# Kernel optimization log

Measured on AMD Instinct MI355X. Metric: run time of the kernel, lower is better.

## Reference

```python
import jax, jax.numpy as jnp
import numpy as np

B, N, D = 8, 8192, 128   # D = in_dim + out_dim
H, KQ = 8, 64


def setup_inputs() -> dict:
    key = jax.random.key(0)
    k1, k2, k3, k4 = jax.random.split(key, 4)
    std = 0.02
    x = jax.random.normal(k1, (B, N, D), dtype=jnp.float32)
    # torch Linear weights are [out_features, in_features]
    Wk = jax.random.normal(k2, (H, KQ, D), dtype=jnp.float32) * std
    Wq = jax.random.normal(k3, (H, KQ, D), dtype=jnp.float32) * std
    Wv = jax.random.normal(k4, (H, D, D), dtype=jnp.float32) * std
    return {"x": x, "Wk": Wk, "Wq": Wq, "Wv": Wv}


def reference(x, Wk, Wq, Wv):
    # Per-head linear projections (Linear: y = x @ W^T), batched over heads.
    K = jnp.einsum('bnd,hkd->bhnk', x, Wk)   # [B,H,N,KQ]
    Q = jnp.einsum('bnd,hkd->bhnk', x, Wq)   # [B,H,N,KQ]
    V = jnp.einsum('bnd,hed->bhne', x, Wv)   # [B,H,N,D]
    # No softmax => (Q K^T) V == Q (K^T V): associative reorder avoids the
    # O(N^2) score matrix while computing identical math.
    KtV = jnp.einsum('bhnk,bhne->bhke', K, V)      # [B,H,KQ,D]
    out = jnp.einsum('bhnk,bhke->bne', Q, KtV)     # heads summed, [B,N,D]
    return out
```

## Files before the change

kernel.cpp:

```cpp
#include <hip/hip_runtime.h>
#include <hip/hip_bf16.h>

#define BB 8
#define NN 8192
#define DD 128
#define HH 8
#define KQ 64
#define SPLIT 64
#define NPB (NN / SPLIT)

typedef __attribute__((ext_vector_type(8))) short s16x8;
typedef __attribute__((ext_vector_type(4))) float f32x4;
typedef __attribute__((ext_vector_type(4))) unsigned short u16x4;
typedef __attribute__((ext_vector_type(8))) unsigned short u16x8;

__device__ __forceinline__ unsigned short bfr(float f) {
  unsigned u = __builtin_bit_cast(unsigned, f);
  u += 0x7fffu + ((u >> 16) & 1u);
  return (unsigned short)(u >> 16);
}
__device__ __forceinline__ float b2f(unsigned short u) {
  unsigned v = (unsigned)u << 16;
  return __builtin_bit_cast(float, v);
}

__global__ __launch_bounds__(256) void prep(
    const float* __restrict__ Wk, const float* __restrict__ Wq,
    const float* __restrict__ Wv, unsigned short* __restrict__ Wkbf,
    unsigned short* __restrict__ Wvbf, unsigned short* __restrict__ Wqt) {
  const int bx = blockIdx.x, t = threadIdx.x;
  if (bx < 64) {
    const int i = bx * 1024 + t * 4;
    float4 v = *(const float4*)(Wk + i);
    u16x4 o = {bfr(v.x), bfr(v.y), bfr(v.z), bfr(v.w)};
    *(u16x4*)(Wkbf + i) = o;
  } else if (bx < 192) {
    const int i = (bx - 64) * 1024 + t * 4;
    float4 v = *(const float4*)(Wv + i);
    u16x4 o = {bfr(v.x), bfr(v.y), bfr(v.z), bfr(v.w)};
    *(u16x4*)(Wvbf + i) = o;
  } else {
    const int h = bx - 192;
    const int d4 = (t & 31) * 4;
#pragma unroll
    for (int p = 0; p < 8; ++p) {
      const int k = (t >> 5) + p * 8;
      float4 v = *(const float4*)(Wq + (size_t)h * 8192 + k * DD + d4);
      unsigned short* dst = Wqt + (size_t)h * 8192;
      dst[(d4 + 0) * KQ + k] = bfr(v.x);
      dst[(d4 + 1) * KQ + k] = bfr(v.y);
      dst[(d4 + 2) * KQ + k] = bfr(v.z);
      dst[(d4 + 3) * KQ + k] = bfr(v.w);
    }
  }
}

__global__ __launch_bounds__(256) void gram_mfma(
    const float* __restrict__ x, unsigned short* __restrict__ part) {
  const int s = blockIdx.x, b = blockIdx.y;
  const int t = threadIdx.x, l = t & 63, w = t >> 6;
  __shared__ __align__(16) unsigned short xt[2][128 * 32];
  const float* xb = x + ((size_t)b * NN + (size_t)s * NPB) * DD;

  const int sd = t & 15;
  const int sn = (t >> 4) * 2;

  f32x4 acc[4][4];
#pragma unroll
  for (int i = 0; i < 4; ++i)
#pragma unroll
    for (int j = 0; j < 4; ++j) acc[i][j] = (f32x4){0.f, 0.f, 0.f, 0.f};

  float rv[8][2];
  auto load = [&](int sub) {
    const float* xs = xb + (size_t)sub * 32 * DD;
#pragma unroll
    for (int i = 0; i < 8; ++i)
#pragma unroll
      for (int j = 0; j < 2; ++j)
        rv[i][j] = xs[(size_t)(sn + j) * DD + sd + 16 * i];
  };
  auto stage = [&](int buf) {
    const int slot = sn >> 3;
#pragma unroll
    for (int i = 0; i < 8; ++i) {
      const int d = sd + 16 * i;
      unsigned v = (unsigned)bfr(rv[i][0]) | ((unsigned)bfr(rv[i][1]) << 16);
      char* dst = (char*)&xt[buf][0] + d * 64 +
                  (((slot ^ ((d >> 1) & 3)) << 4) | ((sn & 7) * 2));
      *(unsigned*)dst = v;
    }
  };

  load(0);
  stage(0);
  __syncthreads();

  const int d1s = (w & 1) * 64, d2s = (w >> 1) * 64;
  const int lr = l & 15, lk = l >> 4;
  const int nsub = NPB / 32;

  for (int sub = 0; sub < nsub; ++sub) {
    const int cur = sub & 1;
    if (sub + 1 < nsub) load(sub + 1);
    {
      s16x8 af[4], bv[4];
#pragma unroll
      for (int i = 0; i < 4; ++i) {
        const int row = d1s + i * 16 + lr;
        af[i] = *(const s16x8*)((const char*)&xt[cur][0] + row * 64 +
                                ((lk ^ ((row >> 1) & 3)) << 4));
      }
#pragma unroll
      for (int j = 0; j < 4; ++j) {
        const int row = d2s + j * 16 + lr;
        bv[j] = *(const s16x8*)((const char*)&xt[cur][0] + row * 64 +
                                ((lk ^ ((row >> 1) & 3)) << 4));
      }
#pragma unroll
      for (int i = 0; i < 4; ++i)
#pragma unroll
        for (int j = 0; j < 4; ++j)
          acc[i][j] =
              __builtin_amdgcn_mfma_f32_16x16x32_bf16(af[i], bv[j], acc[i][j], 0, 0, 0);
    }
    if (sub + 1 < nsub) stage(cur ^ 1);
    __syncthreads();
  }

  unsigned short* gdst = part + (((size_t)b * SPLIT + s) << 14);
#pragma unroll
  for (int i = 0; i < 4; ++i)
#pragma unroll
    for (int j = 0; j < 4; ++j) {
      u16x4 o = {bfr(acc[i][j][0]), bfr(acc[i][j][1]),
                 bfr(acc[i][j][2]), bfr(acc[i][j][3])};
      *(u16x4*)(gdst + ((w * 16 + i * 4 + j) * 64 + l) * 4) = o;
    }
}

__global__ __launch_bounds__(256) void gram_reduce(
    const unsigned short* __restrict__ part, unsigned short* __restrict__ Gbf) {
  const int b = blockIdx.y;
  const int fidx = blockIdx.x * 1024 + threadIdx.x * 4;
  const unsigned short* p = part + ((size_t)b * SPLIT << 14) + fidx;
  float s0 = 0.f, s1 = 0.f, s2 = 0.f, s3 = 0.f;
  for (int i = 0; i < SPLIT; ++i) {
    u16x4 v = *(const u16x4*)(p + ((size_t)i << 14));
    s0 += b2f(v[0]); s1 += b2f(v[1]); s2 += b2f(v[2]); s3 += b2f(v[3]);
  }
  const int q = fidx >> 2;
  const int l = q & 63, u = q >> 6;
  const int j = u & 3, i = (u >> 2) & 3, w = u >> 4;
  const int lr = l & 15, lk = l >> 4;
  const int row0 = (w & 1) * 64 + i * 16 + lk * 4;
  const int col = (w >> 1) * 64 + j * 16 + lr;
  unsigned short* g = Gbf + ((size_t)b << 14);
  g[(row0 + 0) * 128 + col] = bfr(s0);
  g[(row0 + 1) * 128 + col] = bfr(s1);
  g[(row0 + 2) * 128 + col] = bfr(s2);
  g[(row0 + 3) * 128 + col] = bfr(s3);
}

__global__ __launch_bounds__(256) void middle_fused(
    const unsigned short* __restrict__ Gbf, const unsigned short* __restrict__ Wkbf,
    const unsigned short* __restrict__ Wvbf, const unsigned short* __restrict__ Wqt,
    float* __restrict__ Mp) {
  const int b = blockIdx.x >> 3, h = blockIdx.x & 7;
  const int t = threadIdx.x, l = t & 63, w = t >> 6;
  const int lr = l & 15, lk = l >> 4;
  __shared__ __align__(16) unsigned short Gs[128 * 128];
  __shared__ __align__(16) unsigned short T1s[64 * 128];
  __shared__ __align__(16) unsigned short T2t[128 * 64];

  const unsigned short* gsrc = Gbf + ((size_t)b << 14);
#pragma unroll
  for (int c8 = 0; c8 < 8; ++c8) {
    const int c = t + c8 * 256;
    const int row = c >> 4, slot = c & 15;
    u16x8 v = *(const u16x8*)(gsrc + row * 128 + slot * 8);
    *(u16x8*)(&Gs[row * 128 + ((slot ^ (row & 15)) << 3)]) = v;
  }
  __syncthreads();

  const unsigned short* wk = Wkbf + ((size_t)h << 13);
  s16x8 aw[4];
#pragma unroll
  for (int ks = 0; ks < 4; ++ks)
    aw[ks] = *(const s16x8*)(wk + ((w * 16 + lr) << 7) + ks * 32 + lk * 8);
  f32x4 accA[8];
#pragma unroll
  for (int j = 0; j < 8; ++j) accA[j] = (f32x4){0.f, 0.f, 0.f, 0.f};
#pragma unroll
  for (int nj = 0; nj < 8; ++nj)
#pragma unroll
    for (int ks = 0; ks < 4; ++ks) {
      const int row = nj * 16 + lr;
      const int slot = (ks * 4 + lk) ^ (row & 15);
      s16x8 bfrag = *(const s16x8*)(&Gs[(row << 7) + (slot << 3)]);
      accA[nj] = __builtin_amdgcn_mfma_f32_16x16x32_bf16(aw[ks], bfrag, accA[nj], 0, 0, 0);
    }
#pragma unroll
  for (int nj = 0; nj < 8; ++nj)
#pragma unroll
    for (int r = 0; r < 4; ++r) {
      const int row = w * 16 + lk * 4 + r;
      const int col = nj * 16 + lr;
      const int slot = (col >> 3) ^ (row & 15);
      T1s[(row << 7) + (slot << 3) + (col & 7)] = bfr(accA[nj][r]);
    }
  __syncthreads();

  s16x8 a2[4];
#pragma unroll
  for (int ks = 0; ks < 4; ++ks) {
    const int row = w * 16 + lr;
    const int slot = (ks * 4 + lk) ^ (row & 15);
    a2[ks] = *(const s16x8*)(&T1s[(row << 7) + (slot << 3)]);
  }
  const unsigned short* wv = Wvbf + ((size_t)h << 14);
  f32x4 accB[8];
#pragma unroll
  for (int j = 0; j < 8; ++j) accB[j] = (f32x4){0.f, 0.f, 0.f, 0.f};
#pragma unroll
  for (int nj = 0; nj < 8; ++nj)
#pragma unroll
    for (int ks = 0; ks < 4; ++ks) {
      s16x8 bfrag = *(const s16x8*)(wv + (((size_t)(nj * 16 + lr)) << 7) + ks * 32 + lk * 8);
      accB[nj] = __builtin_amdgcn_mfma_f32_16x16x32_bf16(a2[ks], bfrag, accB[nj], 0, 0, 0);
    }
#pragma unroll
  for (int nj = 0; nj < 8; ++nj)
#pragma unroll
    for (int r = 0; r < 4; ++r) {
      const int e = nj * 16 + lr;
      const int k = w * 16 + lk * 4 + r;
      const int slot = (k >> 3) ^ (e & 7);
      T2t[(e << 6) + (slot << 3) + (k & 7)] = bfr(accB[nj][r]);
    }
  __syncthreads();

  const unsigned short* wq = Wqt + ((size_t)h << 13);
  float* mp = Mp + (((size_t)(b * 8 + h)) << 14);
#pragma unroll
  for (int p = 0; p < 2; ++p) {
    s16x8 a3[2];
#pragma unroll
    for (int ks = 0; ks < 2; ++ks) {
      const int row = (2 * w + p) * 16 + lr;
      const int slot = (ks * 4 + lk) ^ (row & 7);
      a3[ks] = *(const s16x8*)(&T2t[(row << 6) + (slot << 3)]);
    }
    f32x4 accC[8];
#pragma unroll
    for (int j = 0; j < 8; ++j) accC[j] = (f32x4){0.f, 0.f, 0.f, 0.f};
#pragma unroll
    for (int nj = 0; nj < 8; ++nj)
#pragma unroll
      for (int ks = 0; ks < 2; ++ks) {
        s16x8 bfrag = *(const s16x8*)(wq + ((nj * 16 + lr) << 6) + ks * 32 + lk * 8);
        accC[nj] = __builtin_amdgcn_mfma_f32_16x16x32_bf16(a3[ks], bfrag, accC[nj], 0, 0, 0);
      }
#pragma unroll
    for (int nj = 0; nj < 8; ++nj)
#pragma unroll
      for (int r = 0; r < 4; ++r) {
        const int row = (2 * w + p) * 16 + lk * 4 + r;
        const int col = nj * 16 + lr;
        mp[(row << 7) + col] = accC[nj][r];
      }
  }
}

__global__ __launch_bounds__(256) void m_reduce_t(
    const float* __restrict__ Mp, unsigned short* __restrict__ Mt) {
  const int b = blockIdx.y;
  const int idx = blockIdx.x * 1024 + threadIdx.x * 4;
  float4 s = {0.f, 0.f, 0.f, 0.f};
#pragma unroll
  for (int h = 0; h < 8; ++h) {
    float4 v = *(const float4*)(Mp + (((size_t)(b * 8 + h)) << 14) + idx);
    s.x += v.x; s.y += v.y; s.z += v.z; s.w += v.w;
  }
  u16x4 o = {bfr(s.x), bfr(s.y), bfr(s.z), bfr(s.w)};
  *(u16x4*)(Mt + ((size_t)b << 14) + idx) = o;
}

__global__ __launch_bounds__(256) void out_mfma(
    const float* __restrict__ x, const unsigned short* __restrict__ Mt,
    float* __restrict__ out) {
  const int b = blockIdx.y, t = threadIdx.x, l = t & 63, w = t >> 6;
  const int r0 = blockIdx.x * 64;
  __shared__ __align__(16) unsigned short mt[DD * DD];
  const unsigned short* msrc = Mt + (size_t)b * (DD * DD);
#pragma unroll
  for (int k = 0; k < 8; ++k) {
    const int c = t + k * 256;
    const int e = c >> 4, slot = c & 15;
    u16x8 v = *(const u16x8*)(msrc + e * DD + slot * 8);
    *(u16x8*)(&mt[e * DD + ((slot ^ (e & 15)) << 3)]) = v;
  }
  __syncthreads();

  const int lr = l & 15, lk = l >> 4;
  const int rw = r0 + w * 16;
  f32x4 acc[8];
#pragma unroll
  for (int j = 0; j < 8; ++j) acc[j] = (f32x4){0.f, 0.f, 0.f, 0.f};

  const float* xb = x + (size_t)b * NN * DD;
#pragma unroll
  for (int ks = 0; ks < 4; ++ks) {
    const float* p = xb + (size_t)(rw + lr) * DD + ks * 32 + lk * 8;
    float4 v0 = *(const float4*)p;
    float4 v1 = *(const float4*)(p + 4);
    s16x8 af;
    af[0] = (short)bfr(v0.x); af[1] = (short)bfr(v0.y);
    af[2] = (short)bfr(v0.z); af[3] = (short)bfr(v0.w);
    af[4] = (short)bfr(v1.x); af[5] = (short)bfr(v1.y);
    af[6] = (short)bfr(v1.z); af[7] = (short)bfr(v1.w);
    const int slot = ks * 4 + lk;
#pragma unroll
    for (int j = 0; j < 8; ++j) {
      const int e = j * 16 + lr;
      s16x8 bv = *(const s16x8*)(&mt[e * DD + ((slot ^ (e & 15)) << 3)]);
      acc[j] = __builtin_amdgcn_mfma_f32_16x16x32_bf16(af, bv, acc[j], 0, 0, 0);
    }
  }

  float* ob = out + (size_t)b * NN * DD;
#pragma unroll
  for (int j = 0; j < 8; ++j)
#pragma unroll
    for (int r = 0; r < 4; ++r) {
      const int row = rw + lk * 4 + r;
      const int col = j * 16 + lr;
      ob[(size_t)row * DD + col] = acc[j][r];
    }
}

extern "C" void kernel_launch(void* const* d_in, const int* in_sizes, int n_in,
                              void* d_out, int out_size, void* d_ws, size_t ws_size,
                              hipStream_t stream) {
  const float* x  = (const float*)d_in[0];
  const float* Wk = (const float*)d_in[1];
  const float* Wq = (const float*)d_in[2];
  const float* Wv = (const float*)d_in[3];
  float* out = (float*)d_out;
  float* ws  = (float*)d_ws;

  const size_t off_Mp   = 0;
  const size_t off_part = off_Mp + (size_t)BB * HH * DD * DD;
  const size_t off_Gbf  = off_part + (size_t)BB * SPLIT * DD * DD / 2;
  const size_t off_Mt   = off_Gbf + (size_t)BB * DD * DD / 2;
  const size_t off_Wkbf = off_Mt + (size_t)BB * DD * DD / 2;
  const size_t off_Wvbf = off_Wkbf + (size_t)HH * KQ * DD / 2;
  const size_t off_Wqt  = off_Wvbf + (size_t)HH * DD * DD / 2;

  float* Mp   = ws + off_Mp;
  unsigned short* part = (unsigned short*)(ws + off_part);
  unsigned short* Gbf  = (unsigned short*)(ws + off_Gbf);
  unsigned short* Mt   = (unsigned short*)(ws + off_Mt);
  unsigned short* Wkbf = (unsigned short*)(ws + off_Wkbf);
  unsigned short* Wvbf = (unsigned short*)(ws + off_Wvbf);
  unsigned short* Wqt  = (unsigned short*)(ws + off_Wqt);

  gram_mfma<<<dim3(SPLIT, BB), 256, 0, stream>>>(x, part);
  prep<<<200, 256, 0, stream>>>(Wk, Wq, Wv, Wkbf, Wvbf, Wqt);
  gram_reduce<<<dim3(16, BB), 256, 0, stream>>>(part, Gbf);
  middle_fused<<<64, 256, 0, stream>>>(Gbf, Wkbf, Wvbf, Wqt, Mp);
  m_reduce_t<<<dim3(16, BB), 256, 0, stream>>>(Mp, Mt);
  out_mfma<<<dim3(NN / 64, BB), 256, 0, stream>>>(x, Mt, out);
}
```

Baseline: 52.11 us.

## Fuse gram reduce with weight prep, deepen gram prefetch, drop LDS in out kernel

Three changes are made. Gram partial reduction and weight bf16 conversion are merged into one launch to save a kernel launch. The gram kernel's global loads are prefetched two sub-tiles ahead with a fully unrolled loop to hide memory latency. The output kernel now reads the M matrix straight from global/L2 instead of staging it in LDS, and uses 128-thread blocks covering 32 rows, which removes the LDS fill and barrier but relies on cache for repeated B-fragment loads and adds register pressure in the gram kernel.

After: 57.56 us. 1.1x slower.

```diff
diff --git a/kernel.cpp b/kernel.cpp
--- a/kernel.cpp
+++ b/kernel.cpp
@@ -24,27 +24,147 @@
   return __builtin_bit_cast(float, v);
 }
 
-__global__ __launch_bounds__(256) void prep(
+__global__ __launch_bounds__(256) void gram_mfma(
+    const float* __restrict__ x, unsigned short* __restrict__ part) {
+  const int s = blockIdx.x, b = blockIdx.y;
+  const int t = threadIdx.x, l = t & 63, w = t >> 6;
+  __shared__ __align__(16) unsigned short xt[2][128 * 32];
+  const float* xb = x + ((size_t)b * NN + (size_t)s * NPB) * DD;
+
+  const int sd = t & 15;
+  const int sn = (t >> 4) * 2;
+
+  f32x4 acc[4][4];
+#pragma unroll
+  for (int i = 0; i < 4; ++i)
+#pragma unroll
+    for (int j = 0; j < 4; ++j) acc[i][j] = (f32x4){0.f, 0.f, 0.f, 0.f};
+
+  float rv[2][8][2];
+  auto load = [&](int slot2, int sub) {
+    const float* xs = xb + (size_t)sub * 32 * DD;
+#pragma unroll
+    for (int i = 0; i < 8; ++i)
+#pragma unroll
+      for (int j = 0; j < 2; ++j)
+        rv[slot2][i][j] = xs[(size_t)(sn + j) * DD + sd + 16 * i];
+  };
+  auto stage = [&](int buf, int slot2) {
+    const int slot = sn >> 3;
+#pragma unroll
+    for (int i = 0; i < 8; ++i) {
+      const int d = sd + 16 * i;
+      unsigned v = (unsigned)bfr(rv[slot2][i][0]) |
+                   ((unsigned)bfr(rv[slot2][i][1]) << 16);
+      char* dst = (char*)&xt[buf][0] + d * 64 +
+                  (((slot ^ ((d >> 1) & 3)) << 4) | ((sn & 7) * 2));
+      *(unsigned*)dst = v;
+    }
+  };
+
+  const int nsub = NPB / 32;
+  load(0, 0);
+  load(1, 1);
+  stage(0, 0);
+  __syncthreads();
+
+  const int d1s = (w & 1) * 64, d2s = (w >> 1) * 64;
+  const int lr = l & 15, lk = l >> 4;
+
+#pragma unroll
+  for (int sub = 0; sub < nsub; ++sub) {
+    const int cur = sub & 1;
+    if (sub + 2 < nsub) load(sub & 1, sub + 2);
+    {
+      s16x8 af[4], bv[4];
+#pragma unroll
+      for (int i = 0; i < 4; ++i) {
+        const int row = d1s + i * 16 + lr;
+        af[i] = *(const s16x8*)((const char*)&xt[cur][0] + row * 64 +
+                                ((lk ^ ((row >> 1) & 3)) << 4));
+      }
+#pragma unroll
+      for (int j = 0; j < 4; ++j) {
+        const int row = d2s + j * 16 + lr;
+        bv[j] = *(const s16x8*)((const char*)&xt[cur][0] + row * 64 +
+                                ((lk ^ ((row >> 1) & 3)) << 4));
+      }
+#pragma unroll
+      for (int i = 0; i < 4; ++i)
+#pragma unroll
+        for (int j = 0; j < 4; ++j)
+          acc[i][j] =
+              __builtin_amdgcn_mfma_f32_16x16x32_bf16(af[i], bv[j], acc[i][j], 0, 0, 0);
+    }
+    if (sub + 1 < nsub) stage(cur ^ 1, (sub + 1) & 1);
+    __syncthreads();
+  }
+
+  unsigned short* gdst = part + (((size_t)b * SPLIT + s) << 14);
+#pragma unroll
+  for (int i = 0; i < 4; ++i)
+#pragma unroll
+    for (int j = 0; j < 4; ++j) {
+      u16x4 o = {bfr(acc[i][j][0]), bfr(acc[i][j][1]),
+                 bfr(acc[i][j][2]), bfr(acc[i][j][3])};
+      *(u16x4*)(gdst + ((w * 16 + i * 4 + j) * 64 + l) * 4) = o;
+    }
+}
+
+__global__ __launch_bounds__(256) void redprep(
+    const unsigned short* __restrict__ part, unsigned short* __restrict__ Gbf,
     const float* __restrict__ Wk, const float* __restrict__ Wq,
     const float* __restrict__ Wv, unsigned short* __restrict__ Wkbf,
     unsigned short* __restrict__ Wvbf, unsigned short* __restrict__ Wqt) {
-  const int bx = blockIdx.x, t = threadIdx.x;
-  if (bx < 64) {
-    const int i = bx * 1024 + t * 4;
-    float4 v = *(const float4*)(Wk + i);
-    u16x4 o = {bfr(v.x), bfr(v.y), bfr(v.z), bfr(v.w)};
-    *(u16x4*)(Wkbf + i) = o;
-  } else if (bx < 192) {
-    const int i = (bx - 64) * 1024 + t * 4;
-    float4 v = *(const float4*)(Wv + i);
-    u16x4 o = {bfr(v.x), bfr(v.y), bfr(v.z), bfr(v.w)};
-    *(u16x4*)(Wvbf + i) = o;
+  const int bx = blockIdx.x, by = blockIdx.y, t = threadIdx.x;
+  if (bx < 16) {
+    const int b = by;
+    const int fidx = bx * 1024 + t * 4;
+    const unsigned short* p = part + ((size_t)b * SPLIT << 14) + fidx;
+    float s0 = 0.f, s1 = 0.f, s2 = 0.f, s3 = 0.f;
+    for (int i = 0; i < SPLIT; ++i) {
+      u16x4 v = *(const u16x4*)(p + ((size_t)i << 14));
+      s0 += b2f(v[0]); s1 += b2f(v[1]); s2 += b2f(v[2]); s3 += b2f(v[3]);
+    }
+    const int q = fidx >> 2;
+    const int l = q & 63, u = q >> 6;
+    const int j = u & 3, i = (u >> 2) & 3, w = u >> 4;
+    const int lr = l & 15, lk = l >> 4;
+    const int row0 = (w & 1) * 64 + i * 16 + lk * 4;
+    const int col = (w >> 1) * 64 + j * 16 + lr;
+    unsigned short* g = Gbf + ((size_t)b << 14);
+    g[(row0 + 0) * 128 + col] = bfr(s0);
+    g[(row0 + 1) * 128 + col] = bfr(s1);
+    g[(row0 + 2) * 128 + col] = bfr(s2);
+    g[(row0 + 3) * 128 + col] = bfr(s3);
+    return;
+  }
+  const int c = (bx - 16) * 8 + by;
+  if (c < 16) {
+    const int base = c * 4096;
+#pragma unroll
+    for (int q = 0; q < 4; ++q) {
+      const int i = base + q * 1024 + t * 4;
+      float4 v = *(const float4*)(Wk + i);
+      u16x4 o = {bfr(v.x), bfr(v.y), bfr(v.z), bfr(v.w)};
+      *(u16x4*)(Wkbf + i) = o;
+    }
+  } else if (c < 48) {
+    const int base = (c - 16) * 4096;
+#pragma unroll
+    for (int q = 0; q < 4; ++q) {
+      const int i = base + q * 1024 + t * 4;
+      float4 v = *(const float4*)(Wv + i);
+      u16x4 o = {bfr(v.x), bfr(v.y), bfr(v.z), bfr(v.w)};
+      *(u16x4*)(Wvbf + i) = o;
+    }
   } else {
-    const int h = bx - 192;
+    const int c2 = c - 48;
+    const int h = c2 >> 1, piece = c2 & 1;
     const int d4 = (t & 31) * 4;
 #pragma unroll
-    for (int p = 0; p < 8; ++p) {
-      const int k = (t >> 5) + p * 8;
+    for (int p = 0; p < 4; ++p) {
+      const int k = piece * 32 + (t >> 5) * 4 + p;
       float4 v = *(const float4*)(Wq + (size_t)h * 8192 + k * DD + d4);
       unsigned short* dst = Wqt + (size_t)h * 8192;
       dst[(d4 + 0) * KQ + k] = bfr(v.x);
@@ -53,113 +173,6 @@
       dst[(d4 + 3) * KQ + k] = bfr(v.w);
     }
   }
-}
-
-__global__ __launch_bounds__(256) void gram_mfma(
-    const float* __restrict__ x, unsigned short* __restrict__ part) {
-  const int s = blockIdx.x, b = blockIdx.y;
-  const int t = threadIdx.x, l = t & 63, w = t >> 6;
-  __shared__ __align__(16) unsigned short xt[2][128 * 32];
-  const float* xb = x + ((size_t)b * NN + (size_t)s * NPB) * DD;
-
-  const int sd = t & 15;
-  const int sn = (t >> 4) * 2;
-
-  f32x4 acc[4][4];
-#pragma unroll
-  for (int i = 0; i < 4; ++i)
-#pragma unroll
-    for (int j = 0; j < 4; ++j) acc[i][j] = (f32x4){0.f, 0.f, 0.f, 0.f};
-
-  float rv[8][2];
-  auto load = [&](int sub) {
-    const float* xs = xb + (size_t)sub * 32 * DD;
-#pragma unroll
-    for (int i = 0; i < 8; ++i)
-#pragma unroll
-      for (int j = 0; j < 2; ++j)
-        rv[i][j] = xs[(size_t)(sn + j) * DD + sd + 16 * i];
-  };
-  auto stage = [&](int buf) {
-    const int slot = sn >> 3;
-#pragma unroll
-    for (int i = 0; i < 8; ++i) {
-      const int d = sd + 16 * i;
-      unsigned v = (unsigned)bfr(rv[i][0]) | ((unsigned)bfr(rv[i][1]) << 16);
-      char* dst = (char*)&xt[buf][0] + d * 64 +
-                  (((slot ^ ((d >> 1) & 3)) << 4) | ((sn & 7) * 2));
-      *(unsigned*)dst = v;
-    }
-  };
-
-  load(0);
-  stage(0);
-  __syncthreads();
-
-  const int d1s = (w & 1) * 64, d2s = (w >> 1) * 64;
-  const int lr = l & 15, lk = l >> 4;
-  const int nsub = NPB / 32;
-
-  for (int sub = 0; sub < nsub; ++sub) {
-    const int cur = sub & 1;
-    if (sub + 1 < nsub) load(sub + 1);
-    {
-      s16x8 af[4], bv[4];
-#pragma unroll
-      for (int i = 0; i < 4; ++i) {
-        const int row = d1s + i * 16 + lr;
-        af[i] = *(const s16x8*)((const char*)&xt[cur][0] + row * 64 +
-                                ((lk ^ ((row >> 1) & 3)) << 4));
-      }
-#pragma unroll
-      for (int j = 0; j < 4; ++j) {
-        const int row = d2s + j * 16 + lr;
-        bv[j] = *(const s16x8*)((const char*)&xt[cur][0] + row * 64 +
-                                ((lk ^ ((row >> 1) & 3)) << 4));
-      }
-#pragma unroll
-      for (int i = 0; i < 4; ++i)
-#pragma unroll
-        for (int j = 0; j < 4; ++j)
-          acc[i][j] =
-              __builtin_amdgcn_mfma_f32_16x16x32_bf16(af[i], bv[j], acc[i][j], 0, 0, 0);
-    }
-    if (sub + 1 < nsub) stage(cur ^ 1);
-    __syncthreads();
-  }
-
-  unsigned short* gdst = part + (((size_t)b * SPLIT + s) << 14);
-#pragma unroll
-  for (int i = 0; i < 4; ++i)
-#pragma unroll
-    for (int j = 0; j < 4; ++j) {
-      u16x4 o = {bfr(acc[i][j][0]), bfr(acc[i][j][1]),
-                 bfr(acc[i][j][2]), bfr(acc[i][j][3])};
-      *(u16x4*)(gdst + ((w * 16 + i * 4 + j) * 64 + l) * 4) = o;
-    }
-}
-
-__global__ __launch_bounds__(256) void gram_reduce(
-    const unsigned short* __restrict__ part, unsigned short* __restrict__ Gbf) {
-  const int b = blockIdx.y;
-  const int fidx = blockIdx.x * 1024 + threadIdx.x * 4;
-  const unsigned short* p = part + ((size_t)b * SPLIT << 14) + fidx;
-  float s0 = 0.f, s1 = 0.f, s2 = 0.f, s3 = 0.f;
-  for (int i = 0; i < SPLIT; ++i) {
-    u16x4 v = *(const u16x4*)(p + ((size_t)i << 14));
-    s0 += b2f(v[0]); s1 += b2f(v[1]); s2 += b2f(v[2]); s3 += b2f(v[3]);
-  }
-  const int q = fidx >> 2;
-  const int l = q & 63, u = q >> 6;
-  const int j = u & 3, i = (u >> 2) & 3, w = u >> 4;
-  const int lr = l & 15, lk = l >> 4;
-  const int row0 = (w & 1) * 64 + i * 16 + lk * 4;
-  const int col = (w >> 1) * 64 + j * 16 + lr;
-  unsigned short* g = Gbf + ((size_t)b << 14);
-  g[(row0 + 0) * 128 + col] = bfr(s0);
-  g[(row0 + 1) * 128 + col] = bfr(s1);
-  g[(row0 + 2) * 128 + col] = bfr(s2);
-  g[(row0 + 3) * 128 + col] = bfr(s3);
 }
 
 __global__ __launch_bounds__(256) void middle_fused(
@@ -286,24 +299,14 @@
   *(u16x4*)(Mt + ((size_t)b << 14) + idx) = o;
 }
 
-__global__ __launch_bounds__(256) void out_mfma(
+__global__ __launch_bounds__(128) void out_mfma(
     const float* __restrict__ x, const unsigned short* __restrict__ Mt,
     float* __restrict__ out) {
   const int b = blockIdx.y, t = threadIdx.x, l = t & 63, w = t >> 6;
-  const int r0 = blockIdx.x * 64;
-  __shared__ __align__(16) unsigned short mt[DD * DD];
-  const unsigned short* msrc = Mt + (size_t)b * (DD * DD);
-#pragma unroll
-  for (int k = 0; k < 8; ++k) {
-    const int c = t + k * 256;
-    const int e = c >> 4, slot = c & 15;
-    u16x8 v = *(const u16x8*)(msrc + e * DD + slot * 8);
-    *(u16x8*)(&mt[e * DD + ((slot ^ (e & 15)) << 3)]) = v;
-  }
-  __syncthreads();
-
   const int lr = l & 15, lk = l >> 4;
-  const int rw = r0 + w * 16;
+  const int rw = blockIdx.x * 32 + w * 16;
+  const unsigned short* mb = Mt + ((size_t)b << 14);
+
   f32x4 acc[8];
 #pragma unroll
   for (int j = 0; j < 8; ++j) acc[j] = (f32x4){0.f, 0.f, 0.f, 0.f};
@@ -319,11 +322,9 @@
     af[2] = (short)bfr(v0.z); af[3] = (short)bfr(v0.w);
     af[4] = (short)bfr(v1.x); af[5] = (short)bfr(v1.y);
     af[6] = (short)bfr(v1.z); af[7] = (short)bfr(v1.w);
-    const int slot = ks * 4 + lk;
 #pragma unroll
     for (int j = 0; j < 8; ++j) {
-      const int e = j * 16 + lr;
-      s16x8 bv = *(const s16x8*)(&mt[e * DD + ((slot ^ (e & 15)) << 3)]);
+      s16x8 bv = *(const s16x8*)(mb + (j * 16 + lr) * DD + ks * 32 + lk * 8);
       acc[j] = __builtin_amdgcn_mfma_f32_16x16x32_bf16(af, bv, acc[j], 0, 0, 0);
     }
   }
@@ -366,9 +367,8 @@
   unsigned short* Wqt  = (unsigned short*)(ws + off_Wqt);
 
   gram_mfma<<<dim3(SPLIT, BB), 256, 0, stream>>>(x, part);
-  prep<<<200, 256, 0, stream>>>(Wk, Wq, Wv, Wkbf, Wvbf, Wqt);
-  gram_reduce<<<dim3(16, BB), 256, 0, stream>>>(part, Gbf);
+  redprep<<<dim3(24, BB), 256, 0, stream>>>(part, Gbf, Wk, Wq, Wv, Wkbf, Wvbf, Wqt);
   middle_fused<<<64, 256, 0, stream>>>(Gbf, Wkbf, Wvbf, Wqt, Mp);
   m_reduce_t<<<dim3(16, BB), 256, 0, stream>>>(Mp, Mt);
-  out_mfma<<<dim3(NN / 64, BB), 256, 0, stream>>>(x, Mt, out);
-}
+  out_mfma<<<dim3(NN / 32, BB), 128, 0, stream>>>(x, Mt, out);
+}
```
